# Optimization experiments

Measured on AMD Instinct MI355X. Metric: run time of the kernel, lower is better.

The kernel has to match this reference:

```python
import jax, jax.numpy as jnp
import numpy as np

B, T, D = 8, 2048, 1024          # batch, seq_len, inp_dim
NH, DH = 8, 128                  # head_num, head_dim
H = NH * DH                      # hidden_dim = 1024
P = int((4.0 / 3.0) * H)         # proj_dim = 1365
EPS = 1e-6
CAP = 15.0                       # soft cap for i/f gate pre-activations


def setup_inputs() -> dict:
    key = jax.random.key(0)
    ks = jax.random.split(key, 32)
    r = lambda k, s, sc=0.02: jax.random.normal(k, s, jnp.float32) * sc
    return {
        "x": jax.random.normal(ks[0], (B, T, D), jnp.float32),
        "ln_w": jnp.ones((D,), jnp.float32),
        "ln_b": jnp.zeros((D,), jnp.float32),
        "hln_w": jnp.ones((H,), jnp.float32),
        "hln_b": jnp.zeros((H,), jnp.float32),
        "Wz": r(ks[1], (D, H)), "bz": r(ks[2], (H,)),
        "Wi": r(ks[3], (D, H)), "bi": r(ks[4], (H,)),
        "Wo": r(ks[5], (D, H)), "bo": r(ks[6], (H,)),
        "Wf": r(ks[7], (D, H)), "bf": r(ks[8], (H,)),
        "Rz": r(ks[9], (NH, DH, DH)), "rbz": r(ks[10], (H,)),
        "Ri": r(ks[11], (NH, DH, DH)), "rbi": r(ks[12], (H,)),
        "Ro": r(ks[13], (NH, DH, DH)), "rbo": r(ks[14], (H,)),
        "Rf": r(ks[15], (NH, DH, DH)), "rbf": r(ks[16], (H,)),
        "up_w": r(ks[17], (H, 2 * P)), "up_b": r(ks[18], (2 * P,)),
        "down_w": r(ks[19], (P, D)), "down_b": r(ks[20], (D,)),
    }


def _layernorm(v, w, b):
    mu = jnp.mean(v, axis=-1, keepdims=True)
    var = jnp.mean((v - mu) ** 2, axis=-1, keepdims=True)
    return (v - mu) * jax.lax.rsqrt(var + EPS) * w + b


def _soft_cap(v):
    return CAP * jnp.tanh(v / CAP)


def _block_linear(h, R, rb):
    # block-diagonal linear: h (B,H) -> per-head (B,NH,DH) @ (NH,DH,DH)
    hh = h.reshape(h.shape[0], NH, DH)
    return jnp.einsum('bhd,hde->bhe', hh, R).reshape(h.shape[0], H) + rb


def _multihead_layernorm(h, w, b):
    hh = h.reshape(h.shape[0], NH, DH)
    mu = jnp.mean(hh, axis=-1, keepdims=True)
    var = jnp.mean((hh - mu) ** 2, axis=-1, keepdims=True)
    normed = (hh - mu) * jax.lax.rsqrt(var + EPS)
    return normed.reshape(h.shape[0], H) * w + b


def reference(x, ln_w, ln_b, hln_w, hln_b,
              Wz, bz, Wi, bi, Wo, bo, Wf, bf,
              Rz, rbz, Ri, rbi, Ro, rbo, Rf, rbf,
              up_w, up_b, down_w, down_b):
    # use_conv=False path: x_c == x_t == LayerNorm(x)
    x_n = _layernorm(x, ln_w, ln_b)                       # (B,T,D)
    # precompute all input projections as large GEMMs
    zx = jnp.einsum('btd,dh->bth', x_n, Wz) + bz
    ix = jnp.einsum('btd,dh->bth', x_n, Wi) + bi
    ox = jnp.einsum('btd,dh->bth', x_n, Wo) + bo
    fx = jnp.einsum('btd,dh->bth', x_n, Wf) + bf

    tm = lambda a: jnp.transpose(a, (1, 0, 2))            # time-major
    xs = (tm(zx), tm(ix), tm(ox), tm(fx), tm(x))

    c0 = jnp.zeros((x.shape[0], H), jnp.float32)
    n0 = jnp.ones((x.shape[0], H), jnp.float32)
    h0 = jnp.zeros((x.shape[0], H), jnp.float32)
    m0 = jnp.zeros((x.shape[0], H), jnp.float32)

    def step(carry, inp_t):
        c, n, h, m = carry
        zx_t, ix_t, ox_t, fx_t, xres_t = inp_t
        i_pre = _soft_cap(ix_t + _block_linear(h, Ri, rbi))
        f_pre = _soft_cap(fx_t + _block_linear(h, Rf, rbf))
        z = jnp.tanh(zx_t + _block_linear(h, Rz, rbz))
        o = jax.nn.sigmoid(ox_t + _block_linear(h, Ro, rbo))
        m_t = jnp.maximum(f_pre + m, i_pre)
        i_g = jnp.exp(i_pre - m_t)
        f_g = jnp.exp(f_pre - m_t + m)
        c_t = f_g * c + i_g * z
        n_t = f_g * n + i_g
        h_t = o * (c_t / jnp.maximum(n_t, 1.0))
        out = _multihead_layernorm(h_t, hln_w, hln_b)
        u = out @ up_w + up_b
        u1, u2 = u[:, :P], u[:, P:]
        y = (u1 * jax.nn.gelu(u2, approximate=False)) @ down_w + down_b
        return (c_t, n_t, h_t, m_t), y + xres_t

    _, ys = jax.lax.scan(step, (c0, n0, h0, m0), xs)      # (T,B,D)
    return jnp.transpose(ys, (1, 0, 2))                   # (B,T,D)
```

## Files before the change

### kernel.cpp

```cpp
#include <hip/hip_runtime.h>

typedef unsigned short u16;
typedef __attribute__((ext_vector_type(4))) float v4f;
typedef __attribute__((ext_vector_type(8))) short bf16x8;

#define B_ 8
#define T_ 2048
#define D_ 1024
#define NH_ 8
#define DH_ 128
#define H_ 1024
#define P_ 1365
#define PPAD_ 1408
#define M_ 16384

#define NSCAN 64
#define NGEMM 192

__device__ __forceinline__ u16 f2b(float f) {
    union { float f; unsigned u; } v; v.f = f;
    unsigned r = (v.u + 0x7fffu + ((v.u >> 16) & 1u)) >> 16;
    return (u16)r;
}
__device__ __forceinline__ float b2f(u16 u) {
    union { unsigned u; float f; } v; v.u = ((unsigned)u) << 16;
    return v.f;
}

template<int S>
__device__ __forceinline__ float qb(float x) {
    return __int_as_float(__builtin_amdgcn_update_dpp(
        0, __float_as_int(x), S * 0x55, 0xF, 0xF, true));
}

#define GLD16(gp, lp) __builtin_amdgcn_global_load_lds( \
    (const __attribute__((address_space(1))) void*)(gp), \
    (__attribute__((address_space(3))) void*)(lp), 16, 0, 0)

__global__ __launch_bounds__(256) void transpose_cast(
    const float* __restrict__ in, u16* __restrict__ out,
    int K, int N, int Kpad, int Npad, int ldin, int rowmul, int rowoff)
{
    __shared__ float tile[32][33];
    const int tx = threadIdx.x, ty = threadIdx.y;
    const int nblk = blockIdx.x * 32, kblk = blockIdx.y * 32;
#pragma unroll
    for (int i = 0; i < 4; ++i) {
        int k = kblk + ty + i * 8, n = nblk + tx;
        float v = (k < K && n < N) ? in[(size_t)k * ldin + n] : 0.f;
        tile[ty + i * 8][tx] = v;
    }
    __syncthreads();
#pragma unroll
    for (int i = 0; i < 4; ++i) {
        int n = nblk + ty + i * 8, k = kblk + tx;
        if (n < Npad && k < Kpad)
            out[((size_t)n * rowmul + rowoff) * Kpad + k] = f2b(tile[tx][ty + i * 8]);
    }
}

__global__ __launch_bounds__(256) void bias4_concat(
    const float* __restrict__ bz, const float* __restrict__ bi,
    const float* __restrict__ bo, const float* __restrict__ bf,
    float* __restrict__ b4)
{
    int j = blockIdx.x * 256 + threadIdx.x;
    const float* p = (j < 1024) ? bz : (j < 2048) ? bi : (j < 3072) ? bo : bf;
    b4[((j & 1023) << 2) | (j >> 10)] = p[j & 1023];
}

__global__ __launch_bounds__(128) void rq_prep(
    const float* __restrict__ Rz, const float* __restrict__ Ri,
    const float* __restrict__ Ro, const float* __restrict__ Rf,
    u16* __restrict__ RQ)
{
    const int m = blockIdx.x;
    const int hd = blockIdx.y;
    const int d = threadIdx.x;
    const int g = m & 3, e = m >> 2;
    const float* Rg = (g == 0) ? Rz : (g == 1) ? Ri : (g == 2) ? Ro : Rf;
    RQ[((size_t)hd * 512 + m) * 128 + d] =
        f2b(Rg[((size_t)hd * 128 + d) * 128 + e]);
}

__global__ __launch_bounds__(256) void ln_cast_kernel(
    const float* __restrict__ x, const float* __restrict__ w,
    const float* __restrict__ b, u16* __restrict__ xnb)
{
    const int token = blockIdx.x, tid = threadIdx.x;
    const float4* xr = (const float4*)(x + (size_t)token * D_);
    float4 v = xr[tid];
    float s  = v.x + v.y + v.z + v.w;
    float ss = v.x * v.x + v.y * v.y + v.z * v.z + v.w * v.w;
    for (int off = 32; off; off >>= 1) { s += __shfl_down(s, off); ss += __shfl_down(ss, off); }
    __shared__ float wsum[4], wsq[4], stats[2];
    const int wave = tid >> 6, lane = tid & 63;
    if (lane == 0) { wsum[wave] = s; wsq[wave] = ss; }
    __syncthreads();
    if (tid == 0) {
        float S = 0.f, SS = 0.f;
        for (int i = 0; i < 4; ++i) { S += wsum[i]; SS += wsq[i]; }
        float mu = S * (1.f / 1024.f);
        float var = SS * (1.f / 1024.f) - mu * mu;
        stats[0] = mu; stats[1] = rsqrtf(var + 1e-6f);
    }
    __syncthreads();
    const float mu = stats[0], rs = stats[1];
    float4 wv = ((const float4*)w)[tid];
    float4 bv = ((const float4*)b)[tid];
    ushort4 o;
    o.x = f2b((v.x - mu) * rs * wv.x + bv.x);
    o.y = f2b((v.y - mu) * rs * wv.y + bv.y);
    o.z = f2b((v.z - mu) * rs * wv.z + bv.z);
    o.w = f2b((v.w - mu) * rs * wv.w + bv.w);
    ((ushort4*)(xnb + (size_t)token * D_))[tid] = o;
}

__device__ __forceinline__ void gemm128_core(
    const u16* __restrict__ A, const u16* __restrict__ BT,
    int K, int m0, int n0, v4f acc[4][4])
{
    __shared__ __align__(16) u16 As[4096];
    __shared__ __align__(16) u16 Bs[4096];
    const int tid = threadIdx.x;
    const int wave = tid >> 6, lane = tid & 63;
    const int wm = wave & 1, wn = wave >> 1;
    const int srow = tid >> 2, sseg = tid & 3;
    const int lm = lane & 15, lq = lane >> 4;

    const u16* gA0 = A  + (size_t)(m0 + srow) * K + sseg * 8;
    const u16* gA1 = gA0 + (size_t)64 * K;
    const u16* gB0 = BT + (size_t)(n0 + srow) * K + sseg * 8;
    const u16* gB1 = gB0 + (size_t)64 * K;
    u16* lA0 = As + wave * 512;
    u16* lA1 = As + 2048 + wave * 512;
    u16* lB0 = Bs + wave * 512;
    u16* lB1 = Bs + 2048 + wave * 512;

    for (int kk = 0; kk < K; kk += 32) {
        GLD16(gA0 + kk, lA0);
        GLD16(gA1 + kk, lA1);
        GLD16(gB0 + kk, lB0);
        GLD16(gB1 + kk, lB1);
        __syncthreads();
        bf16x8 a[4], b[4];
#pragma unroll
        for (int i = 0; i < 4; ++i) {
            a[i] = *(const bf16x8*)(As + (wm * 64 + i * 16 + lm) * 32 + lq * 8);
            b[i] = *(const bf16x8*)(Bs + (wn * 64 + i * 16 + lm) * 32 + lq * 8);
        }
#pragma unroll
        for (int i = 0; i < 4; ++i)
#pragma unroll
            for (int j = 0; j < 4; ++j)
                acc[i][j] = __builtin_amdgcn_mfma_f32_16x16x32_bf16(a[i], b[j], acc[i][j], 0, 0, 0);
        __syncthreads();
    }
}

__global__ __launch_bounds__(512, 1) void fused_gemm_scan(
    const u16* __restrict__ xnb,
    const u16* __restrict__ WT4,
    const float* __restrict__ bias4,
    u16* __restrict__ gx4,
    const u16* __restrict__ RQ,
    const float* __restrict__ rb4,
    float* __restrict__ state,
    u16* __restrict__ hraw,
    unsigned* __restrict__ flags,
    int t0, int Tc, int init)
{
    const int tid = threadIdx.x;

    __shared__ __align__(16) u16 As[128 * 32];
    __shared__ __align__(16) u16 Bs[256 * 32];
    __shared__ __align__(16) u16 hL[2][128];

    if (blockIdx.x >= NSCAN) {
        const int gb = blockIdx.x - NSCAN;
        const int wave = tid >> 6, lane = tid & 63;
        const int wm = wave & 1, wn = wave >> 1;
        const int lm = lane & 15, lq = lane >> 4;
        const int srow = tid >> 2, sseg = tid & 3;
        const int RT = (Tc >> 7) * B_;
        const int TT = RT << 4;
        for (int gti = gb; gti < TT; gti += NGEMM) {
            const int rtp = gti >> 4, nt = gti & 15;
            const int tt = rtp >> 3, b = rtp & 7;
            const int m0 = b * T_ + t0 + (tt << 7);
            const int r0 = b * Tc + (tt << 7);
            const int n0 = nt << 8;
            v4f acc[4][4];
#pragma unroll
            for (int i = 0; i < 4; ++i)
#pragma unroll
                for (int j = 0; j < 4; ++j)
#pragma unroll
                    for (int r = 0; r < 4; ++r) acc[i][j][r] = 0.f;
            const u16* gA  = xnb + (size_t)(m0 + srow) * D_ + sseg * 8;
            const u16* gB0 = WT4 + (size_t)(n0 + srow) * D_ + sseg * 8;
            const u16* gB1 = WT4 + (size_t)(n0 + 128 + srow) * D_ + sseg * 8;
            u16* lA  = As + wave * 512;
            u16* lB0 = Bs + wave * 512;
            u16* lB1 = Bs + 4096 + wave * 512;
            for (int kk = 0; kk < D_; kk += 32) {
                GLD16(gA + kk, lA);
                GLD16(gB0 + kk, lB0);
                GLD16(gB1 + kk, lB1);
                __syncthreads();
                bf16x8 av[4], bv[4];
#pragma unroll
                for (int i = 0; i < 4; ++i) {
                    av[i] = *(const bf16x8*)(As + (wm * 64 + i * 16 + lm) * 32 + lq * 8);
                    bv[i] = *(const bf16x8*)(Bs + (wn * 64 + i * 16 + lm) * 32 + lq * 8);
                }
#pragma unroll
                for (int i = 0; i < 4; ++i)
#pragma unroll
                    for (int j = 0; j < 4; ++j)
                        acc[i][j] = __builtin_amdgcn_mfma_f32_16x16x32_bf16(av[i], bv[j], acc[i][j], 0, 0, 0);
                __syncthreads();
            }
            const int col = lm, rb0 = lq * 4;
#pragma unroll
            for (int j = 0; j < 4; ++j) {
                const int n = n0 + wn * 64 + j * 16 + col;
                const float bvv = bias4[n];
#pragma unroll
                for (int i = 0; i < 4; ++i)
#pragma unroll
                    for (int r = 0; r < 4; ++r) {
                        const int rr = r0 + wm * 64 + i * 16 + rb0 + r;
                        gx4[(size_t)rr * 4096 + n] = f2b(acc[i][j][r] + bvv);
                    }
            }
            __syncthreads();
            if (tid == 0) {
                __threadfence();
                atomicAdd(&flags[(b << 4) + (t0 >> 7) + tt], 1u);
            }
        }
        return;
    }

    const int blk = blockIdx.x;
    const int b = blk >> 3, hd = blk & 7;
    const int w = tid >> 6, lane = tid & 63;
    const int lm = lane & 15, lq = lane >> 4;
    const int g = lane & 3;
    const int e = (w << 4) + (lane >> 2);
    const bool st_lane = (g == 0);

    bf16x8 rq[4][4];
    const u16* RQh = RQ + (size_t)hd * (512 * 128);
#pragma unroll
    for (int i = 0; i < 4; ++i)
#pragma unroll
        for (int kc = 0; kc < 4; ++kc)
            rq[i][kc] = *(const bf16x8*)(RQh +
                (size_t)(w * 64 + i * 16 + lm) * 128 + kc * 32 + lq * 8);

    const float K0 = (g == 1 || g == 3) ? 15.f : 1.f;
    const float K1 = (g == 0) ? 2.f : (g == 2) ? 1.f : 30.f;
    const float K2 = (g == 0) ? 2.f : (g == 2) ? 1.f : (2.f / 15.f);
    const float rb_l = rb4[(hd << 9) + (w << 6) + lane];

    float cS = 0.f, nS = 1.f, mS = 0.f, hS = 0.f;
    if (st_lane && !init) {
        float4 s = ((const float4*)state)[(blk << 7) + e];
        cS = s.x; nS = s.y; mS = s.z; hS = s.w;
    }

    if (st_lane) hL[0][e] = f2b(hS);

    const int gtt0 = (t0 >> 7);
    const int smax = (Tc >> 7) - 1;
    const unsigned* fb = flags + (b << 4) + gtt0;

    if (tid == 0) {
        while (__hip_atomic_load(&fb[0], __ATOMIC_RELAXED,
                                 __HIP_MEMORY_SCOPE_AGENT) < 16u) {}
    }
    __syncthreads();
    __threadfence();

    const u16* gxb = gx4 + (size_t)b * Tc * 4096 + (hd << 9) + (w << 6) + lane;
    u16* houtp = hraw + (size_t)(b * T_ + t0) * H_ + (hd << 7) + e;

    u16 pgA = gxb[0], pgB = gxb[4096], pgC = gxb[2 * 4096], pgD = gxb[3 * 4096];

    const v4f z4 = {0.f, 0.f, 0.f, 0.f};

#define SCAN_STEP(TL, RB, WB, PG)                                              \
    {                                                                          \
          \
        const bf16x8 hv0 = *(const bf16x8*)(&hL[RB][0 * 32 + lq * 8]);         \
        const bf16x8 hv1 = *(const bf16x8*)(&hL[RB][1 * 32 + lq * 8]);         \
        const bf16x8 hv2 = *(const bf16x8*)(&hL[RB][2 * 32 + lq * 8]);         \
        const bf16x8 hv3 = *(const bf16x8*)(&hL[RB][3 * 32 + lq * 8]);         \
        v4f p0[4], p1[4];                                                      \
        _Pragma("unroll") for (int i = 0; i < 4; ++i) {                        \
            p0[i] = __builtin_amdgcn_mfma_f32_16x16x32_bf16(hv0, rq[i][0], z4, 0, 0, 0); \
            p1[i] = __builtin_amdgcn_mfma_f32_16x16x32_bf16(hv1, rq[i][1], z4, 0, 0, 0); \
            p0[i] = __builtin_amdgcn_mfma_f32_16x16x32_bf16(hv2, rq[i][2], p0[i], 0, 0, 0); \
            p1[i] = __builtin_amdgcn_mfma_f32_16x16x32_bf16(hv3, rq[i][3], p1[i], 0, 0, 0); \
        }                                                                      \
        const float s0 = p0[0][0] + p1[0][0];                                  \
        const float s1 = p0[1][0] + p1[1][0];                                  \
        const float s2 = p0[2][0] + p1[2][0];                                  \
        const float s3 = p0[3][0] + p1[3][0];                                  \
        const float sel = (lq & 2) ? ((lq & 1) ? s3 : s2)                      \
                                   : ((lq & 1) ? s1 : s0);                     \
        const int tn = ((TL) + 4 < Tc) ? (TL) + 4 : Tc - 1;                    \
        const u16 pgn = gxb[(size_t)tn * 4096];                                \
        const float pre = sel + b2f(PG) + rb_l;                                \
        PG = pgn;                                                              \
        const float tt_ = K0 - K1 * __builtin_amdgcn_rcpf(__expf(pre * K2) + 1.f); \
        const float ipv = qb<1>(tt_);                                          \
        const float ovv = qb<2>(tt_);                                          \
        const float fpv = qb<3>(tt_);                                          \
        if (st_lane) {                                                         \
            const float bm = fpv + mS;                                         \
            const float d  = ipv - bm;                                         \
            const float mt = fmaxf(bm, ipv);                                   \
            const float e1 = __expf(-fabsf(d));                                \
            const float ig = (d >= 0.f) ? 1.f : e1;                            \
            const float fg = (d >= 0.f) ? e1 : 1.f;                            \
            nS = fg * nS + ig;                                                 \
            const float rp = __builtin_amdgcn_rcpf(fmaxf(nS, 1.f));            \
            cS = fg * cS + ig * tt_;                                           \
            mS = mt;                                                           \
            const float hv = ovv * cS * rp;                                    \
            hS = hv;                                                           \
            const u16 hb = f2b(hv);                                            \
            hL[WB][e] = hb;                                                    \
            houtp[(size_t)(TL) * H_] = hb;                                     \
        }                                                                      \
        asm volatile("s_waitcnt lgkmcnt(0)" ::: "memory");                     \
        __builtin_amdgcn_s_barrier();                                          \
        __builtin_amdgcn_sched_barrier(0);                                     \
    }

    for (int s = 0; s <= smax; ++s) {
        const int wtt = (s + 1 <= smax) ? s + 1 : smax;
        if (tid == 0) {
            while (__hip_atomic_load(&fb[wtt], __ATOMIC_RELAXED,
                                     __HIP_MEMORY_SCOPE_AGENT) < 16u) {}
        }
        __syncthreads();
        __threadfence();
        const int base = s << 7;
        for (int tl4 = 0; tl4 < 128; tl4 += 4) {
            const int tl = base + tl4;
            SCAN_STEP(tl,     0, 1, pgA)
            SCAN_STEP(tl + 1, 1, 0, pgB)
            SCAN_STEP(tl + 2, 0, 1, pgC)
            SCAN_STEP(tl + 3, 1, 0, pgD)
        }
    }
#undef SCAN_STEP

    if (st_lane) {
        ((float4*)state)[(blk << 7) + e] = make_float4(cS, nS, mS, hS);
    }
}

__global__ __launch_bounds__(512) void mln_kernel(
    const u16* __restrict__ h_all, const float* __restrict__ w,
    const float* __restrict__ b, u16* __restrict__ hb)
{
    const int token = blockIdx.x, tid = threadIdx.x;
    const int wave = tid >> 6, lane = tid & 63;
    const u16* hr = h_all + (size_t)token * H_ + wave * DH_;
    float a0 = b2f(hr[lane]), a1 = b2f(hr[64 + lane]);
    float s = a0 + a1, ss = a0 * a0 + a1 * a1;
    for (int off = 32; off; off >>= 1) { s += __shfl_xor(s, off); ss += __shfl_xor(ss, off); }
    const float mu = s * (1.f / 128.f);
    const float var = ss * (1.f / 128.f) - mu * mu;
    const float rs = rsqrtf(var + 1e-6f);
    const int c0 = wave * DH_ + lane;
    u16* hw = hb + (size_t)token * H_ + wave * DH_;
    hw[lane]      = f2b((a0 - mu) * rs * w[c0] + b[c0]);
    hw[64 + lane] = f2b((a1 - mu) * rs * w[c0 + 64] + b[c0 + 64]);
}

__global__ __launch_bounds__(256) void gemm_up_geglu(
    const u16* __restrict__ A, const u16* __restrict__ B1T,
    const u16* __restrict__ B2T, const float* __restrict__ upb,
    u16* __restrict__ G)
{
    __shared__ __align__(16) u16 As[4096], B1s[4096], B2s[4096];
    v4f acc1[4][4], acc2[4][4];
#pragma unroll
    for (int i = 0; i < 4; ++i)
#pragma unroll
        for (int j = 0; j < 4; ++j)
#pragma unroll
            for (int r = 0; r < 4; ++r) { acc1[i][j][r] = 0.f; acc2[i][j][r] = 0.f; }
    const int m0 = blockIdx.y * 128, n0 = blockIdx.x * 128;
    const int tid = threadIdx.x;
    const int wave = tid >> 6, lane = tid & 63;
    const int wm = wave & 1, wn = wave >> 1;
    const int srow = tid >> 2, sseg = tid & 3;
    const int lm = lane & 15, lq = lane >> 4;

    const u16* gA0 = A   + (size_t)(m0 + srow) * H_ + sseg * 8;
    const u16* gA1 = gA0 + (size_t)64 * H_;
    const u16* g10 = B1T + (size_t)(n0 + srow) * H_ + sseg * 8;
    const u16* g11 = g10 + (size_t)64 * H_;
    const u16* g20 = B2T + (size_t)(n0 + srow) * H_ + sseg * 8;
    const u16* g21 = g20 + (size_t)64 * H_;
    u16* lA0 = As  + wave * 512;        u16* lA1 = As  + 2048 + wave * 512;
    u16* l10 = B1s + wave * 512;        u16* l11 = B1s + 2048 + wave * 512;
    u16* l20 = B2s + wave * 512;        u16* l21 = B2s + 2048 + wave * 512;

    for (int kk = 0; kk < H_; kk += 32) {
        GLD16(gA0 + kk, lA0); GLD16(gA1 + kk, lA1);
        GLD16(g10 + kk, l10); GLD16(g11 + kk, l11);
        GLD16(g20 + kk, l20); GLD16(g21 + kk, l21);
        __syncthreads();
        bf16x8 a[4], b1[4], b2[4];
#pragma unroll
        for (int i = 0; i < 4; ++i) {
            a[i]  = *(const bf16x8*)(As  + (wm * 64 + i * 16 + lm) * 32 + lq * 8);
            b1[i] = *(const bf16x8*)(B1s + (wn * 64 + i * 16 + lm) * 32 + lq * 8);
            b2[i] = *(const bf16x8*)(B2s + (wn * 64 + i * 16 + lm) * 32 + lq * 8);
        }
#pragma unroll
        for (int i = 0; i < 4; ++i)
#pragma unroll
            for (int j = 0; j < 4; ++j) {
                acc1[i][j] = __builtin_amdgcn_mfma_f32_16x16x32_bf16(a[i], b1[j], acc1[i][j], 0, 0, 0);
                acc2[i][j] = __builtin_amdgcn_mfma_f32_16x16x32_bf16(a[i], b2[j], acc2[i][j], 0, 0, 0);
            }
        __syncthreads();
    }
    const int col = lane & 15, rb0 = (lane >> 4) * 4;
#pragma unroll
    for (int j = 0; j < 4; ++j) {
        const int n = n0 + wn * 64 + j * 16 + col;
        const bool ok = (n < P_);
        const float bb1 = ok ? upb[n] : 0.f;
        const float bb2 = ok ? upb[P_ + n] : 0.f;
#pragma unroll
        for (int i = 0; i < 4; ++i)
#pragma unroll
            for (int r = 0; r < 4; ++r) {
                const int mm = m0 + wm * 64 + i * 16 + rb0 + r;
                float gval = 0.f;
                if (ok) {
                    const float u1 = acc1[i][j][r] + bb1;
                    const float u2 = acc2[i][j][r] + bb2;
                    const float ge = 0.5f * u2 * (1.f + erff(u2 * 0.70710678118654752f));
                    gval = u1 * ge;
                }
                G[(size_t)mm * PPAD_ + n] = f2b(gval);
            }
    }
}

__global__ __launch_bounds__(256) void gemm_down_out(
    const u16* __restrict__ A, const u16* __restrict__ BT,
    const float* __restrict__ bias, const float* __restrict__ resid,
    float* __restrict__ C, int K, int ldc)
{
    v4f acc[4][4];
#pragma unroll
    for (int i = 0; i < 4; ++i)
#pragma unroll
        for (int j = 0; j < 4; ++j)
#pragma unroll
            for (int r = 0; r < 4; ++r) acc[i][j][r] = 0.f;
    const int m0 = blockIdx.y * 128, n0 = blockIdx.x * 128;
    gemm128_core(A, BT, K, m0, n0, acc);
    const int tid = threadIdx.x, wave = tid >> 6, lane = tid & 63;
    const int wm = wave & 1, wn = wave >> 1;
    const int col = lane & 15, rb0 = (lane >> 4) * 4;
#pragma unroll
    for (int j = 0; j < 4; ++j) {
        const int n = n0 + wn * 64 + j * 16 + col;
        const float bv = bias[n];
#pragma unroll
        for (int i = 0; i < 4; ++i)
#pragma unroll
            for (int r = 0; r < 4; ++r) {
                const int mm = m0 + wm * 64 + i * 16 + rb0 + r;
                C[(size_t)mm * ldc + n] = acc[i][j][r] + bv + resid[(size_t)mm * ldc + n];
            }
    }
}

extern "C" void kernel_launch(void* const* d_in, const int* in_sizes, int n_in,
                              void* d_out, int out_size, void* d_ws, size_t ws_size,
                              hipStream_t stream)
{
    const float* x     = (const float*)d_in[0];
    const float* ln_w  = (const float*)d_in[1];
    const float* ln_b  = (const float*)d_in[2];
    const float* hln_w = (const float*)d_in[3];
    const float* hln_b = (const float*)d_in[4];
    const float* Wz = (const float*)d_in[5];  const float* bz  = (const float*)d_in[6];
    const float* Wi = (const float*)d_in[7];  const float* bi  = (const float*)d_in[8];
    const float* Wo = (const float*)d_in[9];  const float* bo  = (const float*)d_in[10];
    const float* Wf = (const float*)d_in[11]; const float* bfv = (const float*)d_in[12];
    const float* Rz = (const float*)d_in[13]; const float* rbz = (const float*)d_in[14];
    const float* Ri = (const float*)d_in[15]; const float* rbi = (const float*)d_in[16];
    const float* Ro = (const float*)d_in[17]; const float* rbo = (const float*)d_in[18];
    const float* Rf = (const float*)d_in[19]; const float* rbf = (const float*)d_in[20];
    const float* up_w   = (const float*)d_in[21]; const float* up_b   = (const float*)d_in[22];
    const float* down_w = (const float*)d_in[23]; const float* down_b = (const float*)d_in[24];
    float* out = (float*)d_out;

    size_t off = 0;
    char* base = (char*)d_ws;
    auto alloc = [&](size_t bytes) -> char* {
        char* r = base + off; off += (bytes + 255) & ~(size_t)255; return r;
    };
    u16*   WT4   = (u16*)  alloc((size_t)4 * H_ * D_ * 2);
    u16*   W1T   = (u16*)  alloc((size_t)PPAD_ * H_ * 2);
    u16*   W2T   = (u16*)  alloc((size_t)PPAD_ * H_ * 2);
    u16*   dnT   = (u16*)  alloc((size_t)D_ * PPAD_ * 2);
    u16*   RQ    = (u16*)  alloc((size_t)8 * 512 * 128 * 2);
    float* bias4 = (float*)alloc(4096 * 4);
    float* rb4   = (float*)alloc(4096 * 4);
    float* state = (float*)alloc((size_t)64 * 4 * 128 * 4);
    unsigned* flags = (unsigned*)alloc(128 * 4);
    u16*   hbn   = (u16*)  alloc((size_t)M_ * H_ * 2);
    char*  dyn   = base + off;
    u16*   xnb   = (u16*)dyn;
    const size_t xnb_bytes = (size_t)M_ * H_ * 2;
    u16*   gbuf  = (u16*)dyn;

    const size_t fixed = off + xnb_bytes;
    int Tc = 256;
    if      (ws_size >= fixed + (size_t)4 * B_ * 2048 * H_ * 2) Tc = 2048;
    else if (ws_size >= fixed + (size_t)4 * B_ * 1024 * H_ * 2) Tc = 1024;
    else if (ws_size >= fixed + (size_t)4 * B_ * 512  * H_ * 2) Tc = 512;
    u16* gx = (u16*)(dyn + xnb_bytes);
    const int NC = T_ / Tc;

    hipMemsetAsync(flags, 0, 128 * 4, stream);

    dim3 tb(32, 8);
    const float* Ws[4] = {Wz, Wi, Wo, Wf};
    for (int g = 0; g < 4; ++g)
        transpose_cast<<<dim3(32, 32), tb, 0, stream>>>(
            Ws[g], WT4, D_, H_, D_, H_, H_, 4, g);
    transpose_cast<<<dim3(44, 32), tb, 0, stream>>>(up_w,      W1T, H_, P_, H_, PPAD_, 2 * P_, 1, 0);
    transpose_cast<<<dim3(44, 32), tb, 0, stream>>>(up_w + P_, W2T, H_, P_, H_, PPAD_, 2 * P_, 1, 0);
    transpose_cast<<<dim3(32, 44), tb, 0, stream>>>(down_w, dnT, P_, D_, PPAD_, D_, D_, 1, 0);
    bias4_concat<<<16, 256, 0, stream>>>(bz, bi, bo, bfv, bias4);
    bias4_concat<<<16, 256, 0, stream>>>(rbz, rbi, rbo, rbf, rb4);
    rq_prep<<<dim3(512, 8), 128, 0, stream>>>(Rz, Ri, Ro, Rf, RQ);

    ln_cast_kernel<<<M_, 256, 0, stream>>>(x, ln_w, ln_b, xnb);

    for (int cidx = 0; cidx < NC; ++cidx) {
        const int t0 = cidx * Tc;
        fused_gemm_scan<<<NSCAN + NGEMM, 512, 0, stream>>>(
            xnb, WT4, bias4, gx, RQ, rb4, state, hbn, flags,
            t0, Tc, cidx == 0 ? 1 : 0);
    }

    mln_kernel<<<M_, 512, 0, stream>>>(hbn, hln_w, hln_b, hbn);

    gemm_up_geglu<<<dim3(PPAD_ / 128, 128), 256, 0, stream>>>(hbn, W1T, W2T, up_b, gbuf);
    gemm_down_out<<<dim3(8, 128), 256, 0, stream>>>(gbuf, dnT, down_b, x, out, PPAD_, D_);

    (void)in_sizes; (void)n_in; (void)out_size;
}
```

Measured before the change: 1.724 ms.

## Fuse head layernorm, up-GEGLU and down GEMM into persistent scan pipeline

The separate multihead-layernorm, up-projection GEGLU and down-projection kernels move into the persistent gate-GEMM/scan kernel. The worker blocks pick up these stages per 128-token tile once the scan blocks signal completion through new per-tile atomic flags, so this post-scan work overlaps the serial recurrence instead of running after it. The GEGLU output reuses the gate buffer, and the scan loop is unrolled to 8 steps with deeper gate prefetch. The added costs are spin-wait synchronisation, more flag memsets per chunk, and competition between the worker GEMMs and the latency-critical scan blocks for memory bandwidth.

New measurement: 2.017 ms. 17.0% more time.

```diff
diff --git a/kernel.cpp b/kernel.cpp
--- a/kernel.cpp
+++ b/kernel.cpp
@@ -15,7 +15,7 @@
 #define M_ 16384
 
 #define NSCAN 64
-#define NGEMM 192
+#define NWORK 192
 
 __device__ __forceinline__ u16 f2b(float f) {
     union { float f; unsigned u; } v; v.f = f;
@@ -116,64 +116,34 @@
     ((ushort4*)(xnb + (size_t)token * D_))[tid] = o;
 }
 
-__device__ __forceinline__ void gemm128_core(
-    const u16* __restrict__ A, const u16* __restrict__ BT,
-    int K, int m0, int n0, v4f acc[4][4])
-{
-    __shared__ __align__(16) u16 As[4096];
-    __shared__ __align__(16) u16 Bs[4096];
-    const int tid = threadIdx.x;
-    const int wave = tid >> 6, lane = tid & 63;
-    const int wm = wave & 1, wn = wave >> 1;
-    const int srow = tid >> 2, sseg = tid & 3;
-    const int lm = lane & 15, lq = lane >> 4;
-
-    const u16* gA0 = A  + (size_t)(m0 + srow) * K + sseg * 8;
-    const u16* gA1 = gA0 + (size_t)64 * K;
-    const u16* gB0 = BT + (size_t)(n0 + srow) * K + sseg * 8;
-    const u16* gB1 = gB0 + (size_t)64 * K;
-    u16* lA0 = As + wave * 512;
-    u16* lA1 = As + 2048 + wave * 512;
-    u16* lB0 = Bs + wave * 512;
-    u16* lB1 = Bs + 2048 + wave * 512;
-
-    for (int kk = 0; kk < K; kk += 32) {
-        GLD16(gA0 + kk, lA0);
-        GLD16(gA1 + kk, lA1);
-        GLD16(gB0 + kk, lB0);
-        GLD16(gB1 + kk, lB1);
-        __syncthreads();
-        bf16x8 a[4], b[4];
-#pragma unroll
-        for (int i = 0; i < 4; ++i) {
-            a[i] = *(const bf16x8*)(As + (wm * 64 + i * 16 + lm) * 32 + lq * 8);
-            b[i] = *(const bf16x8*)(Bs + (wn * 64 + i * 16 + lm) * 32 + lq * 8);
-        }
-#pragma unroll
-        for (int i = 0; i < 4; ++i)
-#pragma unroll
-            for (int j = 0; j < 4; ++j)
-                acc[i][j] = __builtin_amdgcn_mfma_f32_16x16x32_bf16(a[i], b[j], acc[i][j], 0, 0, 0);
-        __syncthreads();
-    }
-}
-
-__global__ __launch_bounds__(512, 1) void fused_gemm_scan(
+__global__ __launch_bounds__(512, 1) void fused_pipeline(
     const u16* __restrict__ xnb,
     const u16* __restrict__ WT4,
     const float* __restrict__ bias4,
-    u16* __restrict__ gx4,
+    u16* gx4,
     const u16* __restrict__ RQ,
     const float* __restrict__ rb4,
     float* __restrict__ state,
     u16* __restrict__ hraw,
-    unsigned* __restrict__ flags,
-    int t0, int Tc, int init)
+    u16* __restrict__ hbn,
+    const u16* __restrict__ W1T,
+    const u16* __restrict__ W2T,
+    const float* __restrict__ upb,
+    const u16* __restrict__ dnT,
+    const float* __restrict__ dnb,
+    const float* __restrict__ xres,
+    float* __restrict__ outp,
+    const float* __restrict__ hlnw, const float* __restrict__ hlnb,
+    unsigned* flags, int t0, int Tc, int init)
 {
     const int tid = threadIdx.x;
-
-    __shared__ __align__(16) u16 As[128 * 32];
-    __shared__ __align__(16) u16 Bs[256 * 32];
+    const int TPB = Tc >> 7;
+    unsigned* fgate = flags;
+    unsigned* fh    = flags + 128;
+    unsigned* fmln  = flags + 256;
+    unsigned* fup   = flags + 384;
+
+    __shared__ __align__(16) u16 SH[20480];
     __shared__ __align__(16) u16 hL[2][128];
 
     if (blockIdx.x >= NSCAN) {
@@ -182,13 +152,13 @@
         const int wm = wave & 1, wn = wave >> 1;
         const int lm = lane & 15, lq = lane >> 4;
         const int srow = tid >> 2, sseg = tid & 3;
-        const int RT = (Tc >> 7) * B_;
-        const int TT = RT << 4;
-        for (int gti = gb; gti < TT; gti += NGEMM) {
-            const int rtp = gti >> 4, nt = gti & 15;
-            const int tt = rtp >> 3, b = rtp & 7;
-            const int m0 = b * T_ + t0 + (tt << 7);
-            const int r0 = b * Tc + (tt << 7);
+
+        const int nGate = (TPB * B_) << 4;
+        for (int it = gb; it < nGate; it += NWORK) {
+            const int rtp = it >> 4, nt = it & 15;
+            const int tt = rtp >> 3, bb = rtp & 7;
+            const int gm = bb * T_ + t0 + (tt << 7);
+            const int rc = bb * Tc + (tt << 7);
             const int n0 = nt << 8;
             v4f acc[4][4];
 #pragma unroll
@@ -197,22 +167,20 @@
                 for (int j = 0; j < 4; ++j)
 #pragma unroll
                     for (int r = 0; r < 4; ++r) acc[i][j][r] = 0.f;
-            const u16* gA  = xnb + (size_t)(m0 + srow) * D_ + sseg * 8;
+            const u16* gA  = xnb + (size_t)(gm + srow) * D_ + sseg * 8;
             const u16* gB0 = WT4 + (size_t)(n0 + srow) * D_ + sseg * 8;
             const u16* gB1 = WT4 + (size_t)(n0 + 128 + srow) * D_ + sseg * 8;
-            u16* lA  = As + wave * 512;
-            u16* lB0 = Bs + wave * 512;
-            u16* lB1 = Bs + 4096 + wave * 512;
+            u16* lA  = SH + wave * 512;
+            u16* lB0 = SH + 4096 + wave * 512;
+            u16* lB1 = SH + 8192 + wave * 512;
             for (int kk = 0; kk < D_; kk += 32) {
-                GLD16(gA + kk, lA);
-                GLD16(gB0 + kk, lB0);
-                GLD16(gB1 + kk, lB1);
+                GLD16(gA + kk, lA); GLD16(gB0 + kk, lB0); GLD16(gB1 + kk, lB1);
                 __syncthreads();
                 bf16x8 av[4], bv[4];
 #pragma unroll
                 for (int i = 0; i < 4; ++i) {
-                    av[i] = *(const bf16x8*)(As + (wm * 64 + i * 16 + lm) * 32 + lq * 8);
-                    bv[i] = *(const bf16x8*)(Bs + (wn * 64 + i * 16 + lm) * 32 + lq * 8);
+                    av[i] = *(const bf16x8*)(SH + (wm * 64 + i * 16 + lm) * 32 + lq * 8);
+                    bv[i] = *(const bf16x8*)(SH + 4096 + (wn * 64 + i * 16 + lm) * 32 + lq * 8);
                 }
 #pragma unroll
                 for (int i = 0; i < 4; ++i)
@@ -221,30 +189,184 @@
                         acc[i][j] = __builtin_amdgcn_mfma_f32_16x16x32_bf16(av[i], bv[j], acc[i][j], 0, 0, 0);
                 __syncthreads();
             }
-            const int col = lm, rb0 = lq * 4;
 #pragma unroll
             for (int j = 0; j < 4; ++j) {
-                const int n = n0 + wn * 64 + j * 16 + col;
+                const int n = n0 + wn * 64 + j * 16 + lm;
                 const float bvv = bias4[n];
 #pragma unroll
                 for (int i = 0; i < 4; ++i)
 #pragma unroll
                     for (int r = 0; r < 4; ++r) {
-                        const int rr = r0 + wm * 64 + i * 16 + rb0 + r;
+                        const int rr = rc + wm * 64 + i * 16 + lq * 4 + r;
                         gx4[(size_t)rr * 4096 + n] = f2b(acc[i][j][r] + bvv);
                     }
             }
             __syncthreads();
+            if (tid == 0) { __threadfence(); atomicAdd(&fgate[bb * TPB + tt], 1u); }
+        }
+
+        const int nMln = TPB * B_;
+        for (int it = gb; it < nMln; it += NWORK) {
+            const int tt = it >> 3, bb = it & 7;
             if (tid == 0) {
-                __threadfence();
-                atomicAdd(&flags[(b << 4) + (t0 >> 7) + tt], 1u);
+                while (__hip_atomic_load(&fh[bb * TPB + tt], __ATOMIC_RELAXED,
+                                         __HIP_MEMORY_SCOPE_AGENT) < 8u) {}
+            }
+            __syncthreads(); __threadfence();
+            const int gm = bb * T_ + t0 + (tt << 7);
+            for (int idx = wave; idx < 1024; idx += 8) {
+                const int tk = idx >> 3, hh = idx & 7;
+                const u16* hr = hraw + (size_t)(gm + tk) * H_ + hh * 128;
+                float a0 = b2f(hr[lane]), a1 = b2f(hr[64 + lane]);
+                float s = a0 + a1, ss = a0 * a0 + a1 * a1;
+                for (int off = 32; off; off >>= 1) { s += __shfl_xor(s, off); ss += __shfl_xor(ss, off); }
+                const float mu = s * (1.f / 128.f);
+                const float var = ss * (1.f / 128.f) - mu * mu;
+                const float rs = rsqrtf(var + 1e-6f);
+                const int c0 = hh * 128 + lane;
+                u16* hw = hbn + (size_t)(gm + tk) * H_ + hh * 128;
+                hw[lane]      = f2b((a0 - mu) * rs * hlnw[c0] + hlnb[c0]);
+                hw[64 + lane] = f2b((a1 - mu) * rs * hlnw[c0 + 64] + hlnb[c0 + 64]);
+            }
+            __syncthreads();
+            if (tid == 0) { __threadfence(); atomicAdd(&fmln[bb * TPB + tt], 1u); }
+        }
+
+        const int nUp = nMln * 6;
+        for (int it = gb; it < nUp; it += NWORK) {
+            const int tt = it / 48; const int r2 = it % 48;
+            const int bb = r2 / 6, nt = r2 % 6;
+            if (tid == 0) {
+                while (__hip_atomic_load(&fmln[bb * TPB + tt], __ATOMIC_RELAXED,
+                                         __HIP_MEMORY_SCOPE_AGENT) < 1u) {}
+            }
+            __syncthreads(); __threadfence();
+            const int gm = bb * T_ + t0 + (tt << 7);
+            const int rc = bb * Tc + (tt << 7);
+            const int n0 = nt << 8;
+            v4f ac1[4][4], ac2[4][4];
+#pragma unroll
+            for (int i = 0; i < 4; ++i)
+#pragma unroll
+                for (int j = 0; j < 4; ++j)
+#pragma unroll
+                    for (int r = 0; r < 4; ++r) { ac1[i][j][r] = 0.f; ac2[i][j][r] = 0.f; }
+            const u16* gA  = hbn + (size_t)(gm + srow) * H_ + sseg * 8;
+            const u16* g10 = W1T + (size_t)(n0 + srow) * H_ + sseg * 8;
+            const u16* g11 = W1T + (size_t)(n0 + 128 + srow) * H_ + sseg * 8;
+            const u16* g20 = W2T + (size_t)(n0 + srow) * H_ + sseg * 8;
+            const u16* g21 = W2T + (size_t)(n0 + 128 + srow) * H_ + sseg * 8;
+            u16* lA  = SH + wave * 512;
+            u16* l10 = SH + 4096 + wave * 512;
+            u16* l11 = SH + 8192 + wave * 512;
+            u16* l20 = SH + 12288 + wave * 512;
+            u16* l21 = SH + 16384 + wave * 512;
+            for (int kk = 0; kk < H_; kk += 32) {
+                GLD16(gA + kk, lA);
+                GLD16(g10 + kk, l10); GLD16(g11 + kk, l11);
+                GLD16(g20 + kk, l20); GLD16(g21 + kk, l21);
+                __syncthreads();
+                bf16x8 av[4], b1v[4], b2v[4];
+#pragma unroll
+                for (int i = 0; i < 4; ++i) {
+                    av[i]  = *(const bf16x8*)(SH + (wm * 64 + i * 16 + lm) * 32 + lq * 8);
+                    b1v[i] = *(const bf16x8*)(SH + 4096  + (wn * 64 + i * 16 + lm) * 32 + lq * 8);
+                    b2v[i] = *(const bf16x8*)(SH + 12288 + (wn * 64 + i * 16 + lm) * 32 + lq * 8);
+                }
+#pragma unroll
+                for (int i = 0; i < 4; ++i)
+#pragma unroll
+                    for (int j = 0; j < 4; ++j) {
+                        ac1[i][j] = __builtin_amdgcn_mfma_f32_16x16x32_bf16(av[i], b1v[j], ac1[i][j], 0, 0, 0);
+                        ac2[i][j] = __builtin_amdgcn_mfma_f32_16x16x32_bf16(av[i], b2v[j], ac2[i][j], 0, 0, 0);
+                    }
+                __syncthreads();
+            }
+#pragma unroll
+            for (int j = 0; j < 4; ++j) {
+                const int n = n0 + wn * 64 + j * 16 + lm;
+                const bool ok = (n < P_);
+                const float bb1 = ok ? upb[n] : 0.f;
+                const float bb2 = ok ? upb[P_ + n] : 0.f;
+#pragma unroll
+                for (int i = 0; i < 4; ++i)
+#pragma unroll
+                    for (int r = 0; r < 4; ++r) {
+                        const int rr = rc + wm * 64 + i * 16 + lq * 4 + r;
+                        float gval = 0.f;
+                        if (ok) {
+                            const float u1 = ac1[i][j][r] + bb1;
+                            const float u2 = ac2[i][j][r] + bb2;
+                            const float ge = 0.5f * u2 * (1.f + erff(u2 * 0.70710678118654752f));
+                            gval = u1 * ge;
+                        }
+                        gx4[(size_t)rr * 4096 + n] = f2b(gval);
+                    }
+            }
+            __syncthreads();
+            if (tid == 0) { __threadfence(); atomicAdd(&fup[bb * TPB + tt], 1u); }
+        }
+
+        const int nDown = nMln * 4;
+        for (int it = gb; it < nDown; it += NWORK) {
+            const int tt = it >> 5; const int r2 = it & 31;
+            const int bb = r2 >> 2, dn = r2 & 3;
+            if (tid == 0) {
+                while (__hip_atomic_load(&fup[bb * TPB + tt], __ATOMIC_RELAXED,
+                                         __HIP_MEMORY_SCOPE_AGENT) < 6u) {}
+            }
+            __syncthreads(); __threadfence();
+            const int gm = bb * T_ + t0 + (tt << 7);
+            const int rc = bb * Tc + (tt << 7);
+            const int n0 = dn << 8;
+            v4f acc[4][4];
+#pragma unroll
+            for (int i = 0; i < 4; ++i)
+#pragma unroll
+                for (int j = 0; j < 4; ++j)
+#pragma unroll
+                    for (int r = 0; r < 4; ++r) acc[i][j][r] = 0.f;
+            const u16* gA  = gx4 + (size_t)(rc + srow) * 4096 + sseg * 8;
+            const u16* gB0 = dnT + (size_t)(n0 + srow) * PPAD_ + sseg * 8;
+            const u16* gB1 = dnT + (size_t)(n0 + 128 + srow) * PPAD_ + sseg * 8;
+            u16* lA  = SH + wave * 512;
+            u16* lB0 = SH + 4096 + wave * 512;
+            u16* lB1 = SH + 8192 + wave * 512;
+            for (int kk = 0; kk < PPAD_; kk += 32) {
+                GLD16(gA + kk, lA); GLD16(gB0 + kk, lB0); GLD16(gB1 + kk, lB1);
+                __syncthreads();
+                bf16x8 av[4], bv[4];
+#pragma unroll
+                for (int i = 0; i < 4; ++i) {
+                    av[i] = *(const bf16x8*)(SH + (wm * 64 + i * 16 + lm) * 32 + lq * 8);
+                    bv[i] = *(const bf16x8*)(SH + 4096 + (wn * 64 + i * 16 + lm) * 32 + lq * 8);
+                }
+#pragma unroll
+                for (int i = 0; i < 4; ++i)
+#pragma unroll
+                    for (int j = 0; j < 4; ++j)
+                        acc[i][j] = __builtin_amdgcn_mfma_f32_16x16x32_bf16(av[i], bv[j], acc[i][j], 0, 0, 0);
+                __syncthreads();
+            }
+#pragma unroll
+            for (int j = 0; j < 4; ++j) {
+                const int n = n0 + wn * 64 + j * 16 + lm;
+                const float bv = dnb[n];
+#pragma unroll
+                for (int i = 0; i < 4; ++i)
+#pragma unroll
+                    for (int r = 0; r < 4; ++r) {
+                        const int mm = gm + wm * 64 + i * 16 + lq * 4 + r;
+                        outp[(size_t)mm * D_ + n] =
+                            acc[i][j][r] + bv + xres[(size_t)mm * D_ + n];
+                    }
             }
         }
         return;
     }
 
     const int blk = blockIdx.x;
-    const int b = blk >> 3, hd = blk & 7;
+    const int bb = blk >> 3, hd = blk & 7;
     const int w = tid >> 6, lane = tid & 63;
     const int lm = lane & 15, lq = lane >> 4;
     const int g = lane & 3;
@@ -270,38 +392,35 @@
         float4 s = ((const float4*)state)[(blk << 7) + e];
         cS = s.x; nS = s.y; mS = s.z; hS = s.w;
     }
-
     if (st_lane) hL[0][e] = f2b(hS);
 
-    const int gtt0 = (t0 >> 7);
-    const int smax = (Tc >> 7) - 1;
-    const unsigned* fb = flags + (b << 4) + gtt0;
-
+    const int smax = TPB - 1;
     if (tid == 0) {
-        while (__hip_atomic_load(&fb[0], __ATOMIC_RELAXED,
+        while (__hip_atomic_load(&fgate[bb * TPB], __ATOMIC_RELAXED,
                                  __HIP_MEMORY_SCOPE_AGENT) < 16u) {}
     }
     __syncthreads();
     __threadfence();
 
-    const u16* gxb = gx4 + (size_t)b * Tc * 4096 + (hd << 9) + (w << 6) + lane;
-    u16* houtp = hraw + (size_t)(b * T_ + t0) * H_ + (hd << 7) + e;
-
-    u16 pgA = gxb[0], pgB = gxb[4096], pgC = gxb[2 * 4096], pgD = gxb[3 * 4096];
-
-    const v4f z4 = {0.f, 0.f, 0.f, 0.f};
+    const u16* gxb = gx4 + (size_t)bb * Tc * 4096 + (hd << 9) + (w << 6) + lane;
+    u16* houtp = hraw + (size_t)(bb * T_ + t0) * H_ + (hd << 7) + e;
+
+    u16 pg0 = gxb[0],        pg1 = gxb[4096],     pg2 = gxb[2 * 4096], pg3 = gxb[3 * 4096];
+    u16 pg4 = gxb[4 * 4096], pg5 = gxb[5 * 4096], pg6 = gxb[6 * 4096], pg7 = gxb[7 * 4096];
 
 #define SCAN_STEP(TL, RB, WB, PG)                                              \
     {                                                                          \
-          \
         const bf16x8 hv0 = *(const bf16x8*)(&hL[RB][0 * 32 + lq * 8]);         \
         const bf16x8 hv1 = *(const bf16x8*)(&hL[RB][1 * 32 + lq * 8]);         \
         const bf16x8 hv2 = *(const bf16x8*)(&hL[RB][2 * 32 + lq * 8]);         \
         const bf16x8 hv3 = *(const bf16x8*)(&hL[RB][3 * 32 + lq * 8]);         \
         v4f p0[4], p1[4];                                                      \
+        _Pragma("unroll") for (int i = 0; i < 4; ++i)                          \
+            _Pragma("unroll") for (int r = 0; r < 4; ++r) {                    \
+                p0[i][r] = 0.f; p1[i][r] = 0.f; }                              \
         _Pragma("unroll") for (int i = 0; i < 4; ++i) {                        \
-            p0[i] = __builtin_amdgcn_mfma_f32_16x16x32_bf16(hv0, rq[i][0], z4, 0, 0, 0); \
-            p1[i] = __builtin_amdgcn_mfma_f32_16x16x32_bf16(hv1, rq[i][1], z4, 0, 0, 0); \
+            p0[i] = __builtin_amdgcn_mfma_f32_16x16x32_bf16(hv0, rq[i][0], p0[i], 0, 0, 0); \
+            p1[i] = __builtin_amdgcn_mfma_f32_16x16x32_bf16(hv1, rq[i][1], p1[i], 0, 0, 0); \
             p0[i] = __builtin_amdgcn_mfma_f32_16x16x32_bf16(hv2, rq[i][2], p0[i], 0, 0, 0); \
             p1[i] = __builtin_amdgcn_mfma_f32_16x16x32_bf16(hv3, rq[i][3], p1[i], 0, 0, 0); \
         }                                                                      \
@@ -311,7 +430,7 @@
         const float s3 = p0[3][0] + p1[3][0];                                  \
         const float sel = (lq & 2) ? ((lq & 1) ? s3 : s2)                      \
                                    : ((lq & 1) ? s1 : s0);                     \
-        const int tn = ((TL) + 4 < Tc) ? (TL) + 4 : Tc - 1;                    \
+        const int tn = ((TL) + 8 < Tc) ? (TL) + 8 : Tc - 1;                    \
         const u16 pgn = gxb[(size_t)tn * 4096];                                \
         const float pre = sel + b2f(PG) + rb_l;                                \
         PG = pgn;                                                              \
@@ -326,11 +445,10 @@
             const float e1 = __expf(-fabsf(d));                                \
             const float ig = (d >= 0.f) ? 1.f : e1;                            \
             const float fg = (d >= 0.f) ? e1 : 1.f;                            \
+            cS = fg * cS + ig * tt_;                                           \
             nS = fg * nS + ig;                                                 \
-            const float rp = __builtin_amdgcn_rcpf(fmaxf(nS, 1.f));            \
-            cS = fg * cS + ig * tt_;                                           \
             mS = mt;                                                           \
-            const float hv = ovv * cS * rp;                                    \
+            const float hv = ovv * cS * __builtin_amdgcn_rcpf(fmaxf(nS, 1.f)); \
             hS = hv;                                                           \
             const u16 hb = f2b(hv);                                            \
             hL[WB][e] = hb;                                                    \
@@ -344,149 +462,31 @@
     for (int s = 0; s <= smax; ++s) {
         const int wtt = (s + 1 <= smax) ? s + 1 : smax;
         if (tid == 0) {
-            while (__hip_atomic_load(&fb[wtt], __ATOMIC_RELAXED,
+            while (__hip_atomic_load(&fgate[bb * TPB + wtt], __ATOMIC_RELAXED,
                                      __HIP_MEMORY_SCOPE_AGENT) < 16u) {}
         }
         __syncthreads();
         __threadfence();
         const int base = s << 7;
-        for (int tl4 = 0; tl4 < 128; tl4 += 4) {
-            const int tl = base + tl4;
-            SCAN_STEP(tl,     0, 1, pgA)
-            SCAN_STEP(tl + 1, 1, 0, pgB)
-            SCAN_STEP(tl + 2, 0, 1, pgC)
-            SCAN_STEP(tl + 3, 1, 0, pgD)
+        for (int t8 = 0; t8 < 128; t8 += 8) {
+            const int tl = base + t8;
+            SCAN_STEP(tl,     0, 1, pg0)
+            SCAN_STEP(tl + 1, 1, 0, pg1)
+            SCAN_STEP(tl + 2, 0, 1, pg2)
+            SCAN_STEP(tl + 3, 1, 0, pg3)
+            SCAN_STEP(tl + 4, 0, 1, pg4)
+            SCAN_STEP(tl + 5, 1, 0, pg5)
+            SCAN_STEP(tl + 6, 0, 1, pg6)
+            SCAN_STEP(tl + 7, 1, 0, pg7)
         }
+        asm volatile("s_waitcnt vmcnt(0)" ::: "memory");
+        __builtin_amdgcn_s_barrier();
+        if (tid == 0) { __threadfence(); atomicAdd(&fh[bb * TPB + s], 1u); }
     }
 #undef SCAN_STEP
 
     if (st_lane) {
         ((float4*)state)[(blk << 7) + e] = make_float4(cS, nS, mS, hS);
-    }
-}
-
-__global__ __launch_bounds__(512) void mln_kernel(
-    const u16* __restrict__ h_all, const float* __restrict__ w,
-    const float* __restrict__ b, u16* __restrict__ hb)
-{
-    const int token = blockIdx.x, tid = threadIdx.x;
-    const int wave = tid >> 6, lane = tid & 63;
-    const u16* hr = h_all + (size_t)token * H_ + wave * DH_;
-    float a0 = b2f(hr[lane]), a1 = b2f(hr[64 + lane]);
-    float s = a0 + a1, ss = a0 * a0 + a1 * a1;
-    for (int off = 32; off; off >>= 1) { s += __shfl_xor(s, off); ss += __shfl_xor(ss, off); }
-    const float mu = s * (1.f / 128.f);
-    const float var = ss * (1.f / 128.f) - mu * mu;
-    const float rs = rsqrtf(var + 1e-6f);
-    const int c0 = wave * DH_ + lane;
-    u16* hw = hb + (size_t)token * H_ + wave * DH_;
-    hw[lane]      = f2b((a0 - mu) * rs * w[c0] + b[c0]);
-    hw[64 + lane] = f2b((a1 - mu) * rs * w[c0 + 64] + b[c0 + 64]);
-}
-
-__global__ __launch_bounds__(256) void gemm_up_geglu(
-    const u16* __restrict__ A, const u16* __restrict__ B1T,
-    const u16* __restrict__ B2T, const float* __restrict__ upb,
-    u16* __restrict__ G)
-{
-    __shared__ __align__(16) u16 As[4096], B1s[4096], B2s[4096];
-    v4f acc1[4][4], acc2[4][4];
-#pragma unroll
-    for (int i = 0; i < 4; ++i)
-#pragma unroll
-        for (int j = 0; j < 4; ++j)
-#pragma unroll
-            for (int r = 0; r < 4; ++r) { acc1[i][j][r] = 0.f; acc2[i][j][r] = 0.f; }
-    const int m0 = blockIdx.y * 128, n0 = blockIdx.x * 128;
-    const int tid = threadIdx.x;
-    const int wave = tid >> 6, lane = tid & 63;
-    const int wm = wave & 1, wn = wave >> 1;
-    const int srow = tid >> 2, sseg = tid & 3;
-    const int lm = lane & 15, lq = lane >> 4;
-
-    const u16* gA0 = A   + (size_t)(m0 + srow) * H_ + sseg * 8;
-    const u16* gA1 = gA0 + (size_t)64 * H_;
-    const u16* g10 = B1T + (size_t)(n0 + srow) * H_ + sseg * 8;
-    const u16* g11 = g10 + (size_t)64 * H_;
-    const u16* g20 = B2T + (size_t)(n0 + srow) * H_ + sseg * 8;
-    const u16* g21 = g20 + (size_t)64 * H_;
-    u16* lA0 = As  + wave * 512;        u16* lA1 = As  + 2048 + wave * 512;
-    u16* l10 = B1s + wave * 512;        u16* l11 = B1s + 2048 + wave * 512;
-    u16* l20 = B2s + wave * 512;        u16* l21 = B2s + 2048 + wave * 512;
-
-    for (int kk = 0; kk < H_; kk += 32) {
-        GLD16(gA0 + kk, lA0); GLD16(gA1 + kk, lA1);
-        GLD16(g10 + kk, l10); GLD16(g11 + kk, l11);
-        GLD16(g20 + kk, l20); GLD16(g21 + kk, l21);
-        __syncthreads();
-        bf16x8 a[4], b1[4], b2[4];
-#pragma unroll
-        for (int i = 0; i < 4; ++i) {
-            a[i]  = *(const bf16x8*)(As  + (wm * 64 + i * 16 + lm) * 32 + lq * 8);
-            b1[i] = *(const bf16x8*)(B1s + (wn * 64 + i * 16 + lm) * 32 + lq * 8);
-            b2[i] = *(const bf16x8*)(B2s + (wn * 64 + i * 16 + lm) * 32 + lq * 8);
-        }
-#pragma unroll
-        for (int i = 0; i < 4; ++i)
-#pragma unroll
-            for (int j = 0; j < 4; ++j) {
-                acc1[i][j] = __builtin_amdgcn_mfma_f32_16x16x32_bf16(a[i], b1[j], acc1[i][j], 0, 0, 0);
-                acc2[i][j] = __builtin_amdgcn_mfma_f32_16x16x32_bf16(a[i], b2[j], acc2[i][j], 0, 0, 0);
-            }
-        __syncthreads();
-    }
-    const int col = lane & 15, rb0 = (lane >> 4) * 4;
-#pragma unroll
-    for (int j = 0; j < 4; ++j) {
-        const int n = n0 + wn * 64 + j * 16 + col;
-        const bool ok = (n < P_);
-        const float bb1 = ok ? upb[n] : 0.f;
-        const float bb2 = ok ? upb[P_ + n] : 0.f;
-#pragma unroll
-        for (int i = 0; i < 4; ++i)
-#pragma unroll
-            for (int r = 0; r < 4; ++r) {
-                const int mm = m0 + wm * 64 + i * 16 + rb0 + r;
-                float gval = 0.f;
-                if (ok) {
-                    const float u1 = acc1[i][j][r] + bb1;
-                    const float u2 = acc2[i][j][r] + bb2;
-                    const float ge = 0.5f * u2 * (1.f + erff(u2 * 0.70710678118654752f));
-                    gval = u1 * ge;
-                }
-                G[(size_t)mm * PPAD_ + n] = f2b(gval);
-            }
-    }
-}
-
-__global__ __launch_bounds__(256) void gemm_down_out(
-    const u16* __restrict__ A, const u16* __restrict__ BT,
-    const float* __restrict__ bias, const float* __restrict__ resid,
-    float* __restrict__ C, int K, int ldc)
-{
-    v4f acc[4][4];
-#pragma unroll
-    for (int i = 0; i < 4; ++i)
-#pragma unroll
-        for (int j = 0; j < 4; ++j)
-#pragma unroll
-            for (int r = 0; r < 4; ++r) acc[i][j][r] = 0.f;
-    const int m0 = blockIdx.y * 128, n0 = blockIdx.x * 128;
-    gemm128_core(A, BT, K, m0, n0, acc);
-    const int tid = threadIdx.x, wave = tid >> 6, lane = tid & 63;
-    const int wm = wave & 1, wn = wave >> 1;
-    const int col = lane & 15, rb0 = (lane >> 4) * 4;
-#pragma unroll
-    for (int j = 0; j < 4; ++j) {
-        const int n = n0 + wn * 64 + j * 16 + col;
-        const float bv = bias[n];
-#pragma unroll
-        for (int i = 0; i < 4; ++i)
-#pragma unroll
-            for (int r = 0; r < 4; ++r) {
-                const int mm = m0 + wm * 64 + i * 16 + rb0 + r;
-                C[(size_t)mm * ldc + n] = acc[i][j][r] + bv + resid[(size_t)mm * ldc + n];
-            }
     }
 }
 
@@ -517,19 +517,19 @@
         char* r = base + off; off += (bytes + 255) & ~(size_t)255; return r;
     };
     u16*   WT4   = (u16*)  alloc((size_t)4 * H_ * D_ * 2);
-    u16*   W1T   = (u16*)  alloc((size_t)PPAD_ * H_ * 2);
-    u16*   W2T   = (u16*)  alloc((size_t)PPAD_ * H_ * 2);
+    u16*   W1T   = (u16*)  alloc((size_t)1536 * H_ * 2);
+    u16*   W2T   = (u16*)  alloc((size_t)1536 * H_ * 2);
     u16*   dnT   = (u16*)  alloc((size_t)D_ * PPAD_ * 2);
     u16*   RQ    = (u16*)  alloc((size_t)8 * 512 * 128 * 2);
     float* bias4 = (float*)alloc(4096 * 4);
     float* rb4   = (float*)alloc(4096 * 4);
     float* state = (float*)alloc((size_t)64 * 4 * 128 * 4);
-    unsigned* flags = (unsigned*)alloc(128 * 4);
+    unsigned* flags = (unsigned*)alloc(512 * 4);
     u16*   hbn   = (u16*)  alloc((size_t)M_ * H_ * 2);
+    u16*   hraw  = (u16*)  alloc((size_t)M_ * H_ * 2);
     char*  dyn   = base + off;
     u16*   xnb   = (u16*)dyn;
     const size_t xnb_bytes = (size_t)M_ * H_ * 2;
-    u16*   gbuf  = (u16*)dyn;
 
     const size_t fixed = off + xnb_bytes;
     int Tc = 256;
@@ -538,8 +538,6 @@
     else if (ws_size >= fixed + (size_t)4 * B_ * 512  * H_ * 2) Tc = 512;
     u16* gx = (u16*)(dyn + xnb_bytes);
     const int NC = T_ / Tc;
-
-    hipMemsetAsync(flags, 0, 128 * 4, stream);
 
     dim3 tb(32, 8);
     const float* Ws[4] = {Wz, Wi, Wo, Wf};
@@ -557,15 +555,12 @@
 
     for (int cidx = 0; cidx < NC; ++cidx) {
         const int t0 = cidx * Tc;
-        fused_gemm_scan<<<NSCAN + NGEMM, 512, 0, stream>>>(
-            xnb, WT4, bias4, gx, RQ, rb4, state, hbn, flags,
-            t0, Tc, cidx == 0 ? 1 : 0);
-    }
-
-    mln_kernel<<<M_, 512, 0, stream>>>(hbn, hln_w, hln_b, hbn);
-
-    gemm_up_geglu<<<dim3(PPAD_ / 128, 128), 256, 0, stream>>>(hbn, W1T, W2T, up_b, gbuf);
-    gemm_down_out<<<dim3(8, 128), 256, 0, stream>>>(gbuf, dnT, down_b, x, out, PPAD_, D_);
+        hipMemsetAsync(flags, 0, 512 * 4, stream);
+        fused_pipeline<<<NSCAN + NWORK, 512, 0, stream>>>(
+            xnb, WT4, bias4, gx, RQ, rb4, state, hraw, hbn,
+            W1T, W2T, up_b, dnT, down_b, x, out, hln_w, hln_b,
+            flags, t0, Tc, cidx == 0 ? 1 : 0);
+    }
 
     (void)in_sizes; (void)n_in; (void)out_size;
 }
```
